# Kernel tuning notes

Measured on AMD Instinct MI355X. Metric: run time of the kernel, lower is better.

## Reference

```python
import jax, jax.numpy as jnp
import numpy as np

D_MODEL = 1024
N_HEADS = 16
D_K = D_MODEL // N_HEADS
NEG = -1e9


def setup_inputs() -> dict:
    key = jax.random.key(0)
    ks = jax.random.split(key, 10)
    B, S = 4, 2048
    x = jax.random.normal(ks[0], (B, S, D_MODEL), dtype=jnp.float32)
    mask = jax.random.randint(ks[1], (B, S, S), 0, 2).astype(jnp.bool_)
    sc = 1.0 / np.sqrt(D_MODEL)
    Wq = jax.random.normal(ks[2], (D_MODEL, D_MODEL), dtype=jnp.float32) * sc
    bq = jnp.zeros((D_MODEL,), dtype=jnp.float32)
    Wk = jax.random.normal(ks[3], (D_MODEL, D_MODEL), dtype=jnp.float32) * sc
    bk = jnp.zeros((D_MODEL,), dtype=jnp.float32)
    Wv = jax.random.normal(ks[4], (D_MODEL, D_MODEL), dtype=jnp.float32) * sc
    bv = jnp.zeros((D_MODEL,), dtype=jnp.float32)
    Wo = jax.random.normal(ks[5], (D_MODEL, D_MODEL), dtype=jnp.float32) * sc
    bo = jnp.zeros((D_MODEL,), dtype=jnp.float32)
    return {"x": x, "mask": mask, "Wq": Wq, "bq": bq, "Wk": Wk, "bk": bk,
            "Wv": Wv, "bv": bv, "Wo": Wo, "bo": bo}


def _split_heads(t, B, S):
    # [B,S,d_model] -> [B,H,S,d_k]
    return t.reshape(B, S, N_HEADS, D_K).transpose(0, 2, 1, 3)


def reference(x, mask, Wq, bq, Wk, bk, Wv, bv, Wo, bo):
    B, S, _ = x.shape
    Q = _split_heads(x @ Wq + bq, B, S)
    K = _split_heads(x @ Wk + bk, B, S)
    V = _split_heads(x @ Wv + bv, B, S)
    scale = jnp.sqrt(jnp.float32(D_K))
    scores = jnp.einsum('bhqd,bhkd->bhqk', Q, K) / scale
    scores = jnp.where(mask[:, None, :, :], jnp.float32(NEG), scores)
    attn = jax.nn.softmax(scores, axis=-1)
    ctx = jnp.einsum('bhqk,bhkd->bhqd', attn, V)
    ctx = ctx.transpose(0, 2, 1, 3).reshape(B, S, D_MODEL)
    return ctx @ Wo + bo
```

## Files before the change

### kernel.cpp

```cpp
#include <hip/hip_runtime.h>

#define D_MODEL 1024
#define N_HEADS 16
#define D_K     64
#define BATCH   4
#define SEQ     2048
#define MROWS   (BATCH * SEQ)
#define QSCALE  0.18033688011112042f

typedef __bf16 bf16x8 __attribute__((ext_vector_type(8)));
typedef float  f32x4  __attribute__((ext_vector_type(4)));
typedef float  f32x16 __attribute__((ext_vector_type(16)));
typedef unsigned short ushort8 __attribute__((ext_vector_type(8)));
typedef unsigned short ushort4v __attribute__((ext_vector_type(4)));

#if __has_builtin(__builtin_amdgcn_exp2f)
#define EXP2F(x) __builtin_amdgcn_exp2f(x)
#else
#define EXP2F(x) exp2f(x)
#endif

#define CVT_PK_BF16(d, a, b) \
    asm("v_cvt_pk_bf16_f32 %0, %1, %2" : "=v"(d) : "v"(a), "v"(b))
#define PERMSWAP(a, b) \
    asm("v_permlane32_swap_b32 %0, %1" : "+v"(a), "+v"(b))
#define WAIT_VM(N) asm volatile("s_waitcnt vmcnt(" #N ")" ::: "memory")
#define CFENCE()   asm volatile("" ::: "memory")

__device__ inline unsigned short f2bf(float f) {
    union { float f; unsigned int u; } v; v.f = f;
    unsigned int u = v.u;
    unsigned int r = (u + 0x7fffu + ((u >> 16) & 1u)) >> 16;
    return (unsigned short)r;
}

__device__ inline void load_lds16(const void* g, void* l) {
    __builtin_amdgcn_global_load_lds(
        (const __attribute__((address_space(1))) unsigned int*)g,
        (__attribute__((address_space(3))) unsigned int*)l, 16, 0, 0);
}

__global__ __launch_bounds__(256) void wprep(const float* __restrict__ Wq,
                                             const float* __restrict__ Wk,
                                             const float* __restrict__ Wv,
                                             const float* __restrict__ Wo,
                                             unsigned short* __restrict__ wt) {
    __shared__ __align__(16) unsigned short t[64][65];
    int w  = blockIdx.z;
    const float* W = (w == 0) ? Wq : (w == 1) ? Wk : (w == 2) ? Wv : Wo;
    int k0 = blockIdx.x * 64, n0 = blockIdx.y * 64;
    int tid = threadIdx.x;
    int nl = tid & 63, kq = tid >> 6;
#pragma unroll
    for (int i = 0; i < 16; i++) {
        int kl = kq * 16 + i;
        t[kl][nl] = f2bf(W[(size_t)(k0 + kl) * D_MODEL + n0 + nl]);
    }
    __syncthreads();
    unsigned short* out = wt + (size_t)w * D_MODEL * D_MODEL;
#pragma unroll
    for (int p = 0; p < 2; p++) {
        int nrow = p * 32 + (tid >> 3);
        int c8   = (tid & 7) * 8;
        ushort8 o;
#pragma unroll
        for (int j = 0; j < 8; j++) o[j] = t[c8 + j][nrow];
        *reinterpret_cast<ushort8*>(out + (size_t)(n0 + nrow) * D_MODEL + k0 + c8) = o;
    }
}

__global__ __launch_bounds__(256) void xprep(const float4* __restrict__ x,
                                             unsigned short* __restrict__ xb) {
    int i = blockIdx.x * 256 + threadIdx.x;
    float4 v = x[i];
    ushort4v o;
    o[0] = f2bf(v.x); o[1] = f2bf(v.y); o[2] = f2bf(v.z); o[3] = f2bf(v.w);
    *reinterpret_cast<ushort4v*>(xb + (size_t)i * 4) = o;
}

__global__ __launch_bounds__(256) void mprep(const int* __restrict__ mask,
                                             unsigned long long* __restrict__ mb) {
    int row = blockIdx.x;
    int tid = threadIdx.x;
    int wv  = tid >> 6;
#pragma unroll
    for (int w = 0; w < 8; w++) {
        int col = w * 256 + tid;
        int mval = mask[(size_t)row * SEQ + col];
        unsigned long long bits = __ballot(mval != 0);
        if ((tid & 63) == 0) mb[(size_t)row * 32 + w * 4 + wv] = bits;
    }
}

__global__ __launch_bounds__(256) void qkv_gemm(const unsigned short* __restrict__ xb,
                                                const unsigned short* __restrict__ wt,
                                                const float* __restrict__ bq,
                                                const float* __restrict__ bk,
                                                const float* __restrict__ bvv,
                                                unsigned short* __restrict__ qb,
                                                unsigned short* __restrict__ kb,
                                                unsigned short* __restrict__ vt) {
    __shared__ __align__(16) unsigned short lds_a[128 * 32];
    __shared__ __align__(16) unsigned short lds_b[128 * 32];
    int tid = threadIdx.x;
    int wave = tid >> 6, lane = tid & 63;
    int c = lane & 15, g = lane >> 4;
    int wave_m = (wave & 1) * 64, wave_n = (wave >> 1) * 64;
    int wg = blockIdx.x;
    int swz = (wg & 7) * 192 + (wg >> 3);
    int nblk = (swz % 24) * 128, mblk = (swz / 24) * 128;

    int oct0 = wave * 128 + lane, oct1 = oct0 + 64;
    int ra0 = oct0 >> 2, ga0 = ((oct0 & 3) ^ (ra0 & 3)) * 8;
    int ra1 = oct1 >> 2, ga1 = ((oct1 & 3) ^ (ra1 & 3)) * 8;
    const unsigned short* pa0 = xb + (size_t)(mblk + ra0) * D_MODEL + ga0;
    const unsigned short* pa1 = xb + (size_t)(mblk + ra1) * D_MODEL + ga1;
    const unsigned short* pb0 = wt + (size_t)(nblk + ra0) * D_MODEL + ga0;
    const unsigned short* pb1 = wt + (size_t)(nblk + ra1) * D_MODEL + ga1;
    unsigned short* la0 = lds_a + wave * 1024;
    unsigned short* la1 = la0 + 512;
    unsigned short* lb0 = lds_b + wave * 1024;
    unsigned short* lb1 = lb0 + 512;

    int aoff[4], boff[4];
#pragma unroll
    for (int mi = 0; mi < 4; mi++) {
        int row = wave_m + mi * 16 + c;
        aoff[mi] = (row * 4 + (g ^ (row & 3))) * 16;
    }
#pragma unroll
    for (int ni = 0; ni < 4; ni++) {
        int row = wave_n + ni * 16 + c;
        boff[ni] = (row * 4 + (g ^ (row & 3))) * 16;
    }

    f32x4 acc[4][4];
#pragma unroll
    for (int mi = 0; mi < 4; mi++)
#pragma unroll
        for (int ni = 0; ni < 4; ni++) acc[mi][ni] = f32x4{0.f, 0.f, 0.f, 0.f};

    for (int k0 = 0; k0 < D_MODEL; k0 += 32) {
        load_lds16(pa0 + k0, la0);
        load_lds16(pa1 + k0, la1);
        load_lds16(pb0 + k0, lb0);
        load_lds16(pb1 + k0, lb1);
        __syncthreads();
        bf16x8 af[4], bfr[4];
#pragma unroll
        for (int mi = 0; mi < 4; mi++)
            af[mi] = *reinterpret_cast<const bf16x8*>(reinterpret_cast<const char*>(lds_a) + aoff[mi]);
#pragma unroll
        for (int ni = 0; ni < 4; ni++)
            bfr[ni] = *reinterpret_cast<const bf16x8*>(reinterpret_cast<const char*>(lds_b) + boff[ni]);
#pragma unroll
        for (int mi = 0; mi < 4; mi++)
#pragma unroll
            for (int ni = 0; ni < 4; ni++)
                acc[mi][ni] = __builtin_amdgcn_mfma_f32_16x16x32_bf16(af[mi], bfr[ni], acc[mi][ni], 0, 0, 0);
        __syncthreads();
    }

    int nb = nblk + wave_n;
    int wsel = nb >> 10;
    int h = (nb >> 6) & 15;
    int dk0 = nb & 63;
    int mglob = mblk + wave_m;
    int b = mglob >> 11;
    int s0 = mglob & (SEQ - 1);
    size_t bh = (size_t)(b * N_HEADS + h);
    const float* bias = (wsel == 0) ? bq : (wsel == 1) ? bk : bvv;
    int nn = nb & (D_MODEL - 1);
    float bval[4];
#pragma unroll
    for (int ni = 0; ni < 4; ni++) bval[ni] = bias[nn + ni * 16 + c];
    float oscale = (wsel == 0) ? QSCALE : 1.0f;

    if (wsel < 2) {
        unsigned short* outp = wsel ? kb : qb;
#pragma unroll
        for (int mi = 0; mi < 4; mi++)
#pragma unroll
            for (int ni = 0; ni < 4; ni++) {
                int dk = dk0 + ni * 16 + c;
#pragma unroll
                for (int r = 0; r < 4; r++) {
                    int s = s0 + mi * 16 + g * 4 + r;
                    outp[(bh * SEQ + s) * 64 + dk] = f2bf((acc[mi][ni][r] + bval[ni]) * oscale);
                }
            }
    } else {
#pragma unroll
        for (int mi = 0; mi < 4; mi++)
#pragma unroll
            for (int ni = 0; ni < 4; ni++) {
                int dk = dk0 + ni * 16 + c;
                int s = s0 + mi * 16 + g * 4;
                ushort4v o;
#pragma unroll
                for (int r = 0; r < 4; r++) o[r] = f2bf(acc[mi][ni][r] + bval[ni]);
                *reinterpret_cast<ushort4v*>(vt + (bh * 64 + dk) * SEQ + s) = o;
            }
    }
}

__global__ __launch_bounds__(64, 2) void attn(const unsigned short* __restrict__ qb,
                                              const unsigned short* __restrict__ kb,
                                              const unsigned short* __restrict__ vt,
                                              const unsigned long long* __restrict__ mb,
                                              unsigned short* __restrict__ ctx) {
    __shared__ __align__(16) unsigned char smem[16384];

    int lane = threadIdx.x;
    int q31 = lane & 31, hi = lane >> 5;
    int bid = blockIdx.x;
    int swz = (bid & 7) * 256 + (bid >> 3);
    int bh = swz >> 5;
    int q0 = (swz & 31) * 64;
    int b = bh >> 4, h = bh & 15;
    const unsigned short* qbase = qb + (size_t)bh * SEQ * 64;
    const unsigned short* kbase = kb + (size_t)bh * SEQ * 64;
    const unsigned short* vbase = vt + (size_t)bh * 64 * SEQ;
    const unsigned int* mp0 = (const unsigned int*)mb + ((size_t)b * SEQ + q0 + q31) * 64;
    const unsigned int* mp1 = mp0 + 32 * 64;

    bf16x8 qf[2][4];
#pragma unroll
    for (int t = 0; t < 2; t++) {
        const unsigned short* qr = qbase + (size_t)(q0 + 32 * t + q31) * 64 + hi * 8;
#pragma unroll
        for (int c = 0; c < 4; c++)
            qf[t][c] = *reinterpret_cast<const bf16x8*>(qr + c * 16);
    }

    int srow8 = lane >> 3;
    int j7 = lane & 7;
    int soct = j7 ^ srow8;
    const unsigned short* ksrc[4];
    const unsigned short* vsrc[4];
#pragma unroll
    for (int i = 0; i < 4; i++) {
        ksrc[i] = kbase + (size_t)(8 * i + srow8) * 64 + soct * 8;
        vsrc[i] = vbase + (size_t)(8 * i + srow8 + ((soct >> 2) << 5)) * SEQ + (soct & 3) * 8;
    }

    int kofs[4];
#pragma unroll
    for (int c = 0; c < 4; c++)
        kofs[c] = q31 * 128 + (((hi + 2 * c) ^ (q31 & 7)) * 16);
    int vofs[2][2];
#pragma unroll
    for (int so = 0; so < 2; so++)
#pragma unroll
        for (int cp = 0; cp < 2; cp++)
            vofs[so][cp] = q31 * 128 + (((4 * so + hi + 2 * cp) ^ (q31 & 7)) * 16);

    float lsum[2] = {0.f, 0.f};
    f32x16 po[2][2];
#pragma unroll
    for (int i = 0; i < 16; i++) {
        po[0][0][i] = 0.f; po[0][1][i] = 0.f;
        po[1][0][i] = 0.f; po[1][1][i] = 0.f;
    }

    unsigned int mnx0 = mp0[0], mnx1 = mp1[0];
    CFENCE();
#pragma unroll
    for (int i = 0; i < 4; i++) {
        load_lds16(ksrc[i], smem + i * 1024);
        load_lds16(vsrc[i], smem + 4096 + i * 1024);
    }

    for (int it = 0; it < SEQ / 32; it++) {
        unsigned int w32[2];
        w32[0] = mnx0; w32[1] = mnx1;
        int itn = (it + 1 < SEQ / 32) ? it + 1 : it;
        mnx0 = mp0[itn]; mnx1 = mp1[itn];
        CFENCE();
        unsigned char* bufn = smem + ((it + 1) & 1) * 8192;
#pragma unroll
        for (int i = 0; i < 4; i++) {
            load_lds16(ksrc[i] + (size_t)itn * 2048, bufn + i * 1024);
            load_lds16(vsrc[i] + itn * 32, bufn + 4096 + i * 1024);
        }
        WAIT_VM(10);
        CFENCE();

        const char* lkb = (const char*)(smem + (it & 1) * 8192);
        const char* lvb = lkb + 4096;

        f32x16 sq[2];
#pragma unroll
        for (int i = 0; i < 16; i++) { sq[0][i] = 0.f; sq[1][i] = 0.f; }
        __builtin_amdgcn_s_setprio(1);
#pragma unroll
        for (int c = 0; c < 4; c++) {
            bf16x8 kf = *reinterpret_cast<const bf16x8*>(lkb + kofs[c]);
            sq[0] = __builtin_amdgcn_mfma_f32_32x32x16_bf16(kf, qf[0][c], sq[0], 0, 0, 0);
            sq[1] = __builtin_amdgcn_mfma_f32_32x32x16_bf16(kf, qf[1][c], sq[1], 0, 0, 0);
        }
        __builtin_amdgcn_s_setprio(0);
        union PF { uint4 u; bf16x8 v; };
        PF pf[2][2];
#pragma unroll
        for (int t = 0; t < 2; t++) {
            unsigned int wt_ = ~w32[t];
            float pm[16];
#pragma unroll
            for (int j = 0; j < 4; j++) {
                unsigned int nj = wt_ >> (8 * j + 4 * hi);
#pragma unroll
                for (int e = 0; e < 4; e++) {
                    float p = EXP2F(sq[t][4 * j + e]);
                    unsigned int m = (unsigned int)((int)(nj << (31 - e)) >> 31);
                    unsigned int pu = __float_as_uint(p) & m;
                    pm[4 * j + e] = __uint_as_float(pu);
                    lsum[t] += __uint_as_float(pu);
                }
            }
            unsigned int w[8];
#pragma unroll
            for (int j = 0; j < 4; j++) {
                CVT_PK_BF16(w[2 * j],     pm[4 * j + 0], pm[4 * j + 1]);
                CVT_PK_BF16(w[2 * j + 1], pm[4 * j + 2], pm[4 * j + 3]);
            }
            PERMSWAP(w[0], w[2]); PERMSWAP(w[1], w[3]);
            PERMSWAP(w[4], w[6]); PERMSWAP(w[5], w[7]);
            pf[t][0].u = uint4{w[0], w[1], w[2], w[3]};
            pf[t][1].u = uint4{w[4], w[5], w[6], w[7]};
        }
        __builtin_amdgcn_s_setprio(1);
#pragma unroll
        for (int cp = 0; cp < 2; cp++)
#pragma unroll
            for (int so = 0; so < 2; so++) {
                bf16x8 vf = *reinterpret_cast<const bf16x8*>(lvb + vofs[so][cp]);
                po[0][so] = __builtin_amdgcn_mfma_f32_32x32x16_bf16(vf, pf[0][cp].v, po[0][so], 0, 0, 0);
                po[1][so] = __builtin_amdgcn_mfma_f32_32x32x16_bf16(vf, pf[1][cp].v, po[1][so], 0, 0, 0);
            }
        __builtin_amdgcn_s_setprio(0);
    }

    WAIT_VM(0);

    float inv[2];
#pragma unroll
    for (int t = 0; t < 2; t++) {
        lsum[t] += __shfl_xor(lsum[t], 32);
        inv[t] = 1.f / lsum[t];
    }

    unsigned int* ob = (unsigned int*)smem;
    int csw = 4 * (q31 & 7);
#pragma unroll
    for (int t = 0; t < 2; t++) {
        unsigned int* obr = ob + (32 * t + q31) * 32;
#pragma unroll
        for (int so = 0; so < 2; so++)
#pragma unroll
            for (int j = 0; j < 4; j++) {
                unsigned int w0 = (unsigned int)f2bf(po[t][so][4 * j + 0] * inv[t])
                                | ((unsigned int)f2bf(po[t][so][4 * j + 1] * inv[t]) << 16);
                unsigned int w1 = (unsigned int)f2bf(po[t][so][4 * j + 2] * inv[t])
                                | ((unsigned int)f2bf(po[t][so][4 * j + 3] * inv[t]) << 16);
                int d = (16 * so + 4 * j + 2 * hi) ^ csw;
                uint2 u; u.x = w0; u.y = w1;
                *reinterpret_cast<uint2*>(obr + d) = u;
            }
    }
    __builtin_amdgcn_s_waitcnt(0);
    size_t crow = (size_t)b * SEQ + q0;
    int o = lane & 7, rl = lane >> 3;
#pragma unroll
    for (int i = 0; i < 8; i++) {
        int r = 8 * i + rl;
        uint4 v = *reinterpret_cast<const uint4*>(ob + r * 32 + 4 * (o ^ (r & 7)));
        *reinterpret_cast<uint4*>(ctx + (crow + r) * D_MODEL + h * 64 + o * 8) = v;
    }
}

__global__ __launch_bounds__(256) void oproj(const unsigned short* __restrict__ ctx,
                                             const unsigned short* __restrict__ wt,
                                             const float* __restrict__ bo,
                                             float* __restrict__ out) {
    __shared__ __align__(16) unsigned short lds_a[128 * 32];
    __shared__ __align__(16) unsigned short lds_b[128 * 32];
    int tid = threadIdx.x;
    int wave = tid >> 6, lane = tid & 63;
    int c = lane & 15, g = lane >> 4;
    int wave_m = (wave & 1) * 64, wave_n = (wave >> 1) * 64;
    int wg = blockIdx.x;
    int swz = (wg & 7) * 64 + (wg >> 3);
    int nblk = (swz & 7) * 128, mblk = (swz >> 3) * 128;
    const unsigned short* wo = wt + (size_t)3 * D_MODEL * D_MODEL;

    int oct0 = wave * 128 + lane, oct1 = oct0 + 64;
    int ra0 = oct0 >> 2, ga0 = ((oct0 & 3) ^ (ra0 & 3)) * 8;
    int ra1 = oct1 >> 2, ga1 = ((oct1 & 3) ^ (ra1 & 3)) * 8;
    const unsigned short* pa0 = ctx + (size_t)(mblk + ra0) * D_MODEL + ga0;
    const unsigned short* pa1 = ctx + (size_t)(mblk + ra1) * D_MODEL + ga1;
    const unsigned short* pb0 = wo + (size_t)(nblk + ra0) * D_MODEL + ga0;
    const unsigned short* pb1 = wo + (size_t)(nblk + ra1) * D_MODEL + ga1;
    unsigned short* la0 = lds_a + wave * 1024;
    unsigned short* la1 = la0 + 512;
    unsigned short* lb0 = lds_b + wave * 1024;
    unsigned short* lb1 = lb0 + 512;

    int aoff[4], boff[4];
#pragma unroll
    for (int mi = 0; mi < 4; mi++) {
        int row = wave_m + mi * 16 + c;
        aoff[mi] = (row * 4 + (g ^ (row & 3))) * 16;
    }
#pragma unroll
    for (int ni = 0; ni < 4; ni++) {
        int row = wave_n + ni * 16 + c;
        boff[ni] = (row * 4 + (g ^ (row & 3))) * 16;
    }

    f32x4 acc[4][4];
#pragma unroll
    for (int mi = 0; mi < 4; mi++)
#pragma unroll
        for (int ni = 0; ni < 4; ni++) acc[mi][ni] = f32x4{0.f, 0.f, 0.f, 0.f};

    for (int k0 = 0; k0 < D_MODEL; k0 += 32) {
        load_lds16(pa0 + k0, la0);
        load_lds16(pa1 + k0, la1);
        load_lds16(pb0 + k0, lb0);
        load_lds16(pb1 + k0, lb1);
        __syncthreads();
        bf16x8 af[4], bfr[4];
#pragma unroll
        for (int mi = 0; mi < 4; mi++)
            af[mi] = *reinterpret_cast<const bf16x8*>(reinterpret_cast<const char*>(lds_a) + aoff[mi]);
#pragma unroll
        for (int ni = 0; ni < 4; ni++)
            bfr[ni] = *reinterpret_cast<const bf16x8*>(reinterpret_cast<const char*>(lds_b) + boff[ni]);
#pragma unroll
        for (int mi = 0; mi < 4; mi++)
#pragma unroll
            for (int ni = 0; ni < 4; ni++)
                acc[mi][ni] = __builtin_amdgcn_mfma_f32_16x16x32_bf16(af[mi], bfr[ni], acc[mi][ni], 0, 0, 0);
        __syncthreads();
    }

    float bval[4];
#pragma unroll
    for (int ni = 0; ni < 4; ni++) bval[ni] = bo[nblk + wave_n + ni * 16 + c];
#pragma unroll
    for (int mi = 0; mi < 4; mi++)
#pragma unroll
        for (int ni = 0; ni < 4; ni++) {
            int n = nblk + wave_n + ni * 16 + c;
#pragma unroll
            for (int r = 0; r < 4; r++) {
                int m = mblk + wave_m + mi * 16 + g * 4 + r;
                out[(size_t)m * D_MODEL + n] = acc[mi][ni][r] + bval[ni];
            }
        }
}

extern "C" void kernel_launch(void* const* d_in, const int* in_sizes, int n_in,
                              void* d_out, int out_size, void* d_ws, size_t ws_size,
                              hipStream_t stream) {
    const float* x    = (const float*)d_in[0];
    const int*   mask = (const int*)d_in[1];
    const float* Wq = (const float*)d_in[2];
    const float* bq = (const float*)d_in[3];
    const float* Wk = (const float*)d_in[4];
    const float* bk = (const float*)d_in[5];
    const float* Wv = (const float*)d_in[6];
    const float* bv = (const float*)d_in[7];
    const float* Wo = (const float*)d_in[8];
    const float* bo = (const float*)d_in[9];
    float* out = (float*)d_out;

    char* ws = (char*)d_ws;
    const size_t MB = 1024 * 1024;
    unsigned short* wt  = (unsigned short*)(ws + 0 * MB);
    unsigned short* xb  = (unsigned short*)(ws + 8 * MB);
    unsigned short* qb  = (unsigned short*)(ws + 24 * MB);
    unsigned short* kb  = (unsigned short*)(ws + 40 * MB);
    unsigned short* vt  = (unsigned short*)(ws + 56 * MB);
    unsigned short* ctx = (unsigned short*)(ws + 72 * MB);
    unsigned long long* mb = (unsigned long long*)(ws + 88 * MB);

    wprep<<<dim3(16, 16, 4), 256, 0, stream>>>(Wq, Wk, Wv, Wo, wt);
    xprep<<<dim3(MROWS * D_MODEL / 4 / 256), 256, 0, stream>>>((const float4*)x, xb);
    mprep<<<dim3(MROWS), 256, 0, stream>>>(mask, mb);
    qkv_gemm<<<dim3(1536), 256, 0, stream>>>(xb, wt, bq, bk, bv, qb, kb, vt);
    attn<<<dim3(2048), 64, 0, stream>>>(qb, kb, vt, mb, ctx);
    oproj<<<dim3(512), 256, 0, stream>>>(ctx, wt, bo, out);
}
```

Before: 366.5 us.

## Load K/V fragments directly into registers instead of LDS staging in attention

```diff
diff --git a/kernel.cpp b/kernel.cpp
--- a/kernel.cpp
+++ b/kernel.cpp
@@ -24,7 +24,6 @@
     asm("v_cvt_pk_bf16_f32 %0, %1, %2" : "=v"(d) : "v"(a), "v"(b))
 #define PERMSWAP(a, b) \
     asm("v_permlane32_swap_b32 %0, %1" : "+v"(a), "+v"(b))
-#define WAIT_VM(N) asm volatile("s_waitcnt vmcnt(" #N ")" ::: "memory")
 #define CFENCE()   asm volatile("" ::: "memory")
 
 __device__ inline unsigned short f2bf(float f) {
@@ -204,25 +203,26 @@
     }
 }
 
-__global__ __launch_bounds__(64, 2) void attn(const unsigned short* __restrict__ qb,
-                                              const unsigned short* __restrict__ kb,
-                                              const unsigned short* __restrict__ vt,
-                                              const unsigned long long* __restrict__ mb,
-                                              unsigned short* __restrict__ ctx) {
+__global__ __launch_bounds__(128, 2) void attn(const unsigned short* __restrict__ qb,
+                                               const unsigned short* __restrict__ kb,
+                                               const unsigned short* __restrict__ vt,
+                                               const unsigned long long* __restrict__ mb,
+                                               unsigned short* __restrict__ ctx) {
     __shared__ __align__(16) unsigned char smem[16384];
 
-    int lane = threadIdx.x;
+    int tid = threadIdx.x;
+    int wave = tid >> 6, lane = tid & 63;
     int q31 = lane & 31, hi = lane >> 5;
     int bid = blockIdx.x;
-    int swz = (bid & 7) * 256 + (bid >> 3);
-    int bh = swz >> 5;
-    int q0 = (swz & 31) * 64;
+    int swz = (bid & 7) * 128 + (bid >> 3);
+    int bh = swz >> 4;
+    int q0 = (swz & 15) * 128 + wave * 64;
     int b = bh >> 4, h = bh & 15;
     const unsigned short* qbase = qb + (size_t)bh * SEQ * 64;
     const unsigned short* kbase = kb + (size_t)bh * SEQ * 64;
     const unsigned short* vbase = vt + (size_t)bh * 64 * SEQ;
-    const unsigned int* mp0 = (const unsigned int*)mb + ((size_t)b * SEQ + q0 + q31) * 64;
-    const unsigned int* mp1 = mp0 + 32 * 64;
+    const unsigned long long* mp0 = mb + ((size_t)b * SEQ + q0 + q31) * 32;
+    const unsigned long long* mp1 = mp0 + 1024;
 
     bf16x8 qf[2][4];
 #pragma unroll
@@ -233,27 +233,12 @@
             qf[t][c] = *reinterpret_cast<const bf16x8*>(qr + c * 16);
     }
 
-    int srow8 = lane >> 3;
-    int j7 = lane & 7;
-    int soct = j7 ^ srow8;
-    const unsigned short* ksrc[4];
-    const unsigned short* vsrc[4];
-#pragma unroll
-    for (int i = 0; i < 4; i++) {
-        ksrc[i] = kbase + (size_t)(8 * i + srow8) * 64 + soct * 8;
-        vsrc[i] = vbase + (size_t)(8 * i + srow8 + ((soct >> 2) << 5)) * SEQ + (soct & 3) * 8;
-    }
-
-    int kofs[4];
-#pragma unroll
-    for (int c = 0; c < 4; c++)
-        kofs[c] = q31 * 128 + (((hi + 2 * c) ^ (q31 & 7)) * 16);
-    int vofs[2][2];
-#pragma unroll
-    for (int so = 0; so < 2; so++)
-#pragma unroll
-        for (int cp = 0; cp < 2; cp++)
-            vofs[so][cp] = q31 * 128 + (((4 * so + hi + 2 * cp) ^ (q31 & 7)) * 16);
+    const unsigned short* kpp[2];
+    kpp[0] = kbase + (size_t)(q31) * 64 + hi * 8;
+    kpp[1] = kbase + (size_t)(32 + q31) * 64 + hi * 8;
+    const unsigned short* vp[2];
+    vp[0] = vbase + (size_t)(q31) * SEQ + hi * 8;
+    vp[1] = vbase + (size_t)(32 + q31) * SEQ + hi * 8;
 
     float lsum[2] = {0.f, 0.f};
     f32x16 po[2][2];
@@ -263,48 +248,24 @@
         po[1][0][i] = 0.f; po[1][1][i] = 0.f;
     }
 
-    unsigned int mnx0 = mp0[0], mnx1 = mp1[0];
-    CFENCE();
-#pragma unroll
-    for (int i = 0; i < 4; i++) {
-        load_lds16(ksrc[i], smem + i * 1024);
-        load_lds16(vsrc[i], smem + 4096 + i * 1024);
-    }
-
-    for (int it = 0; it < SEQ / 32; it++) {
-        unsigned int w32[2];
-        w32[0] = mnx0; w32[1] = mnx1;
-        int itn = (it + 1 < SEQ / 32) ? it + 1 : it;
-        mnx0 = mp0[itn]; mnx1 = mp1[itn];
-        CFENCE();
-        unsigned char* bufn = smem + ((it + 1) & 1) * 8192;
-#pragma unroll
-        for (int i = 0; i < 4; i++) {
-            load_lds16(ksrc[i] + (size_t)itn * 2048, bufn + i * 1024);
-            load_lds16(vsrc[i] + itn * 32, bufn + 4096 + i * 1024);
-        }
-        WAIT_VM(10);
-        CFENCE();
-
-        const char* lkb = (const char*)(smem + (it & 1) * 8192);
-        const char* lvb = lkb + 4096;
-
+    union PF { uint4 u; bf16x8 v; };
+
+    unsigned long long w64c[2];
+    auto proc = [&](int s, bf16x8 (&kc)[2][4], bf16x8 (&vf)[2][2]) {
         f32x16 sq[2];
 #pragma unroll
         for (int i = 0; i < 16; i++) { sq[0][i] = 0.f; sq[1][i] = 0.f; }
         __builtin_amdgcn_s_setprio(1);
 #pragma unroll
         for (int c = 0; c < 4; c++) {
-            bf16x8 kf = *reinterpret_cast<const bf16x8*>(lkb + kofs[c]);
-            sq[0] = __builtin_amdgcn_mfma_f32_32x32x16_bf16(kf, qf[0][c], sq[0], 0, 0, 0);
-            sq[1] = __builtin_amdgcn_mfma_f32_32x32x16_bf16(kf, qf[1][c], sq[1], 0, 0, 0);
+            sq[0] = __builtin_amdgcn_mfma_f32_32x32x16_bf16(kc[s][c], qf[0][c], sq[0], 0, 0, 0);
+            sq[1] = __builtin_amdgcn_mfma_f32_32x32x16_bf16(kc[s][c], qf[1][c], sq[1], 0, 0, 0);
         }
         __builtin_amdgcn_s_setprio(0);
-        union PF { uint4 u; bf16x8 v; };
         PF pf[2][2];
 #pragma unroll
         for (int t = 0; t < 2; t++) {
-            unsigned int wt_ = ~w32[t];
+            unsigned int wt_ = ~(unsigned int)(w64c[t] >> (32 * s));
             float pm[16];
 #pragma unroll
             for (int j = 0; j < 4; j++) {
@@ -334,14 +295,55 @@
         for (int cp = 0; cp < 2; cp++)
 #pragma unroll
             for (int so = 0; so < 2; so++) {
-                bf16x8 vf = *reinterpret_cast<const bf16x8*>(lvb + vofs[so][cp]);
-                po[0][so] = __builtin_amdgcn_mfma_f32_32x32x16_bf16(vf, pf[0][cp].v, po[0][so], 0, 0, 0);
-                po[1][so] = __builtin_amdgcn_mfma_f32_32x32x16_bf16(vf, pf[1][cp].v, po[1][so], 0, 0, 0);
+                po[0][so] = __builtin_amdgcn_mfma_f32_32x32x16_bf16(vf[so][cp], pf[0][cp].v, po[0][so], 0, 0, 0);
+                po[1][so] = __builtin_amdgcn_mfma_f32_32x32x16_bf16(vf[so][cp], pf[1][cp].v, po[1][so], 0, 0, 0);
             }
         __builtin_amdgcn_s_setprio(0);
-    }
-
-    WAIT_VM(0);
+    };
+
+    unsigned long long mnx0 = mp0[0], mnx1 = mp1[0];
+    bf16x8 kA[2][4], kB[2][4];
+#pragma unroll
+    for (int s = 0; s < 2; s++)
+#pragma unroll
+        for (int c = 0; c < 4; c++)
+            kA[s][c] = *reinterpret_cast<const bf16x8*>(kpp[s] + 16 * c);
+    kpp[0] += 4096; kpp[1] += 4096;
+
+    auto body = [&](bf16x8 (&kc)[2][4], bf16x8 (&kn)[2][4], int it) {
+        w64c[0] = mnx0; w64c[1] = mnx1;
+        int itn = (it + 1 < 32) ? it + 1 : it;
+        bf16x8 vf0[2][2];
+#pragma unroll
+        for (int so = 0; so < 2; so++)
+#pragma unroll
+            for (int cp = 0; cp < 2; cp++)
+                vf0[so][cp] = *reinterpret_cast<const bf16x8*>(vp[so] + 16 * cp);
+        CFENCE();
+        mnx0 = mp0[itn]; mnx1 = mp1[itn];
+#pragma unroll
+        for (int s = 0; s < 2; s++)
+#pragma unroll
+            for (int c = 0; c < 4; c++)
+                kn[s][c] = *reinterpret_cast<const bf16x8*>(kpp[s] + 16 * c);
+        kpp[0] += 4096; kpp[1] += 4096;
+        CFENCE();
+        proc(0, kc, vf0);
+        bf16x8 vf1[2][2];
+#pragma unroll
+        for (int so = 0; so < 2; so++)
+#pragma unroll
+            for (int cp = 0; cp < 2; cp++)
+                vf1[so][cp] = *reinterpret_cast<const bf16x8*>(vp[so] + 32 + 16 * cp);
+        proc(1, kc, vf1);
+        vp[0] += 64; vp[1] += 64;
+    };
+
+#pragma unroll 1
+    for (int i2 = 0; i2 < 16; i2++) {
+        body(kA, kB, 2 * i2);
+        body(kB, kA, 2 * i2 + 1);
+    }
 
     float inv[2];
 #pragma unroll
@@ -350,7 +352,7 @@
         inv[t] = 1.f / lsum[t];
     }
 
-    unsigned int* ob = (unsigned int*)smem;
+    unsigned int* ob = (unsigned int*)(smem + wave * 8192);
     int csw = 4 * (q31 & 7);
 #pragma unroll
     for (int t = 0; t < 2; t++) {
@@ -490,6 +492,6 @@
     xprep<<<dim3(MROWS * D_MODEL / 4 / 256), 256, 0, stream>>>((const float4*)x, xb);
     mprep<<<dim3(MROWS), 256, 0, stream>>>(mask, mb);
     qkv_gemm<<<dim3(1536), 256, 0, stream>>>(xb, wt, bq, bk, bv, qb, kb, vt);
-    attn<<<dim3(2048), 64, 0, stream>>>(qb, kb, vt, mb, ctx);
+    attn<<<dim3(1024), 128, 0, stream>>>(qb, kb, vt, mb, ctx);
     oproj<<<dim3(512), 256, 0, stream>>>(ctx, wt, bo, out);
 }
```

Measured after the change: 422.8 us. 1.15x slower.
